# Optimization experiments

Measured on AMD Instinct MI355X. Metric: run time of the kernel, lower is better.

The kernel has to match this reference:

```python
import jax, jax.numpy as jnp
import numpy as np

V, D, M, C, L = 100000, 256, 4096, 4096, 32
PAD = 0
EPS = 1e-8  # torch CosineSimilarity default eps


def setup_inputs() -> dict:
    key = jax.random.key(0)
    ks = jax.random.split(key, 6)
    xs = jax.random.randint(ks[0], (1, L), 0, V)
    mems = jax.random.randint(ks[1], (M, L), 0, V)
    ys = jax.random.randint(ks[2], (1, L), 0, V)
    cands = jax.random.randint(ks[3], (C, L), 0, V)
    lt = jax.random.normal(ks[4], (V, D), dtype=jnp.float32) * 0.02
    lt = lt.at[PAD].set(0.0)  # nn.Embedding padding_idx row is zero
    freqs = jax.random.uniform(ks[5], (V,), dtype=jnp.float32, minval=0.05, maxval=1.0)
    return {"xs": xs, "mems": mems, "ys": ys, "cands": cands, "lt": lt, "freqs": freqs}


def _encode(tokens, lt, freqs):
    # Batched Encoder.forward: freq-weighted average of token embeddings.
    # tokens: [N, L] -> [N, D]
    emb = lt[tokens]                       # [N, L, D] gather
    w = freqs[tokens]                      # [N, L]
    w = w / jnp.linalg.norm(w, axis=1, keepdims=True)  # w * (1 / ||w||)
    return jnp.einsum('nl,nld->nd', w, emb)


def reference(xs, mems, ys, cands, lt, freqs):
    xs_emb = _encode(xs, lt, freqs)                                   # [1, D]
    mems_enc = jnp.concatenate([_encode(mems, lt, freqs), xs_emb], 0)  # [M+1, D]
    # cosine similarity of xs_emb (broadcast) against each memory row
    an = jnp.maximum(jnp.linalg.norm(xs_emb, axis=1), EPS)            # [1]
    bn = jnp.maximum(jnp.linalg.norm(mems_enc, axis=1), EPS)          # [M+1]
    cos = (mems_enc @ xs_emb[0]) / (an * bn)                          # [M+1]
    att = jax.nn.softmax(cos)[None, :]                                # [1, M+1]
    lhs_emb = att @ mems_enc                                          # [1, D]
    ys_emb = _encode(ys, lt, freqs)                                   # [1, D]
    cand_emb = _encode(cands, lt, freqs)                              # [C, D]
    # torch.cat of lhs_emb repeated (1 + C) times; ys then cand encodings
    xs_out = jnp.tile(lhs_emb, (cands.shape[0] + 1, 1))               # [C+1, D]
    ys_out = jnp.concatenate([ys_emb, cand_emb], axis=0)              # [C+1, D]
    return xs_out, ys_out
```

## Files before the change

### kernel.cpp

```cpp
#include <hip/hip_runtime.h>

#define V_ 100000
#define D_ 256
#define M_ 4096
#define C_ 4096
#define L_ 32
#define ROWS_MEMS (M_ + 1)
#define NTASK (1 + M_ + 1 + C_)

__global__ __launch_bounds__(256) void encode_all(
    const int* __restrict__ xs, const int* __restrict__ mems,
    const int* __restrict__ ys, const int* __restrict__ cands,
    const float* __restrict__ lt, const float* __restrict__ freqs,
    float* __restrict__ mems_enc,
    float* __restrict__ out_ys)
{
    const int wave = threadIdx.x >> 6;
    const int lane = threadIdx.x & 63;
    const int rt = blockIdx.x * 4 + wave;
    if (rt >= NTASK) return;

    const int* tok_ptr;
    float* dst;
    if (rt == 0) {
        tok_ptr = xs;
        dst = mems_enc + (size_t)M_ * D_;
    } else if (rt <= M_) {
        tok_ptr = mems + (size_t)(rt - 1) * L_;
        dst = mems_enc + (size_t)(rt - 1) * D_;
    } else if (rt == M_ + 1) {
        tok_ptr = ys;
        dst = out_ys;
    } else {
        const int c = rt - (M_ + 2);
        tok_ptr = cands + (size_t)c * L_;
        dst = out_ys + (size_t)(c + 1) * D_;
    }

    int tok = 0;
    float w = 0.0f;
    if (lane < L_) {
        tok = tok_ptr[lane];
        w = freqs[tok];
    }
    float s = w * w;
    #pragma unroll
    for (int off = 32; off >= 1; off >>= 1) s += __shfl_down(s, off, 64);
    const float norm = sqrtf(__shfl(s, 0, 64));
    const float wn = w / norm;

    const int d0 = lane * 4;
    float4 acc = make_float4(0.f, 0.f, 0.f, 0.f);
    #pragma unroll
    for (int l = 0; l < L_; ++l) {
        const int t = __shfl(tok, l, 64);
        const float wl = __shfl(wn, l, 64);
        const float4 v = *reinterpret_cast<const float4*>(lt + (size_t)t * D_ + d0);
        acc.x += wl * v.x;
        acc.y += wl * v.y;
        acc.z += wl * v.z;
        acc.w += wl * v.w;
    }
    *reinterpret_cast<float4*>(dst + d0) = acc;
}

__global__ __launch_bounds__(256) void dots_kernel(
    const float* __restrict__ enc, float* __restrict__ dots,
    float* __restrict__ norms2)
{
    __shared__ float sp[4], sq[4];
    const int i = blockIdx.x;
    const int t = threadIdx.x;
    const float r = enc[(size_t)i * D_ + t];
    const float x = enc[(size_t)M_ * D_ + t];
    float p = r * x;
    float q = r * r;
    #pragma unroll
    for (int off = 32; off >= 1; off >>= 1) {
        p += __shfl_down(p, off, 64);
        q += __shfl_down(q, off, 64);
    }
    const int wave = t >> 6, lane = t & 63;
    if (lane == 0) { sp[wave] = p; sq[wave] = q; }
    __syncthreads();
    if (t == 0) {
        dots[i]   = sp[0] + sp[1] + sp[2] + sp[3];
        norms2[i] = sq[0] + sq[1] + sq[2] + sq[3];
    }
}

__global__ __launch_bounds__(1024) void softmax_kernel(
    const float* __restrict__ dots, const float* __restrict__ norms2,
    float* __restrict__ att)
{
    __shared__ float red[16];
    const int t = threadIdx.x;
    const int wave = t >> 6, lane = t & 63;

    const float an = fmaxf(sqrtf(norms2[M_]), 1e-8f);

    float cosv[5];
    int cnt = 0;
    float mx = -1e30f;
    for (int i = t; i < ROWS_MEMS; i += 1024) {
        const float bn = fmaxf(sqrtf(norms2[i]), 1e-8f);
        const float c = dots[i] / (an * bn);
        cosv[cnt++] = c;
        mx = fmaxf(mx, c);
    }
    #pragma unroll
    for (int off = 32; off >= 1; off >>= 1) mx = fmaxf(mx, __shfl_down(mx, off, 64));
    if (lane == 0) red[wave] = mx;
    __syncthreads();
    if (t < 16) {
        float m = red[t];
        #pragma unroll
        for (int off = 8; off >= 1; off >>= 1) m = fmaxf(m, __shfl_down(m, off, 16));
        if (t == 0) red[0] = m;
    }
    __syncthreads();
    mx = red[0];
    __syncthreads();

    float s = 0.f;
    for (int k = 0; k < cnt; ++k) { cosv[k] = expf(cosv[k] - mx); s += cosv[k]; }
    #pragma unroll
    for (int off = 32; off >= 1; off >>= 1) s += __shfl_down(s, off, 64);
    if (lane == 0) red[wave] = s;
    __syncthreads();
    if (t < 16) {
        float m = red[t];
        #pragma unroll
        for (int off = 8; off >= 1; off >>= 1) m += __shfl_down(m, off, 16);
        if (t == 0) red[0] = m;
    }
    __syncthreads();
    const float inv = 1.0f / red[0];

    cnt = 0;
    for (int i = t; i < ROWS_MEMS; i += 1024) att[i] = cosv[cnt++] * inv;
}

__global__ __launch_bounds__(256) void lhs_kernel(
    const float* __restrict__ enc, const float* __restrict__ att,
    float* __restrict__ lhs)
{
    const int d = threadIdx.x;
    const int i0 = blockIdx.x * 64;
    const int i1 = min(i0 + 64, ROWS_MEMS);
    float acc = 0.f;
    for (int i = i0; i < i1; ++i) acc += att[i] * enc[(size_t)i * D_ + d];
    atomicAdd(&lhs[d], acc);
}

__global__ __launch_bounds__(256) void tile_kernel(
    const float* __restrict__ lhs, float* __restrict__ out_xs)
{
    out_xs[(size_t)blockIdx.x * D_ + threadIdx.x] = lhs[threadIdx.x];
}

extern "C" void kernel_launch(void* const* d_in, const int* in_sizes, int n_in,
                              void* d_out, int out_size, void* d_ws, size_t ws_size,
                              hipStream_t stream) {
    const int*   xs    = (const int*)d_in[0];
    const int*   mems  = (const int*)d_in[1];
    const int*   ys    = (const int*)d_in[2];
    const int*   cands = (const int*)d_in[3];
    const float* lt    = (const float*)d_in[4];
    const float* freqs = (const float*)d_in[5];

    float* out    = (float*)d_out;
    float* out_xs = out;
    float* out_ys = out + (size_t)ROWS_MEMS * D_;

    float* enc    = (float*)d_ws;
    float* dots   = enc + (size_t)ROWS_MEMS * D_;
    float* norms2 = dots + ROWS_MEMS;
    float* att    = norms2 + ROWS_MEMS;
    float* lhs    = att + ROWS_MEMS;

    hipMemsetAsync(lhs, 0, D_ * sizeof(float), stream);

    encode_all<<<(NTASK + 3) / 4, 256, 0, stream>>>(xs, mems, ys, cands, lt, freqs,
                                                    enc, out_ys);
    dots_kernel<<<ROWS_MEMS, 256, 0, stream>>>(enc, dots, norms2);
    softmax_kernel<<<1, 1024, 0, stream>>>(dots, norms2, att);
    lhs_kernel<<<(ROWS_MEMS + 63) / 64, 256, 0, stream>>>(enc, att, lhs);
    tile_kernel<<<ROWS_MEMS, 256, 0, stream>>>(lhs, out_xs);
}
```

Baseline: 208.9 us.

## Fuse cosine scoring and softmax exponent into encoder, drop max-subtraction and atomics

Each memory-row wave recomputes the xs encoding locally and computes the dot product, norms and exp(cos) right after encoding. This removes the separate dots and softmax kernels along with their global round trips. Because cosine values are bounded in [-1,1], the softmax max-subtraction is dropped. Normalization moves into a chunked weighted-sum kernel plus a final tile kernel that divides by the global sum, replacing the atomic accumulation and the memset. The cost is that every memory wave does an extra 32-row gather for xs, and only 16 blocks perform the weighted reduction over 4097 rows, which limits parallelism in that stage.

```diff
diff --git a/kernel.cpp b/kernel.cpp
--- a/kernel.cpp
+++ b/kernel.cpp
@@ -7,156 +7,116 @@
 #define L_ 32
 #define ROWS_MEMS (M_ + 1)
 #define NTASK (1 + M_ + 1 + C_)
+#define NCHUNK 16
 
-__global__ __launch_bounds__(256) void encode_all(
+__device__ __forceinline__ float wave_allreduce_sum(float v) {
+    #pragma unroll
+    for (int off = 32; off >= 1; off >>= 1) v += __shfl_xor(v, off, 64);
+    return v;
+}
+
+__global__ __launch_bounds__(256) void encode_att(
     const int* __restrict__ xs, const int* __restrict__ mems,
     const int* __restrict__ ys, const int* __restrict__ cands,
     const float* __restrict__ lt, const float* __restrict__ freqs,
-    float* __restrict__ mems_enc,
+    float* __restrict__ enc,
+    float* __restrict__ att,
     float* __restrict__ out_ys)
 {
     const int wave = threadIdx.x >> 6;
     const int lane = threadIdx.x & 63;
     const int rt = blockIdx.x * 4 + wave;
     if (rt >= NTASK) return;
+    const int d0 = lane * 4;
 
-    const int* tok_ptr;
-    float* dst;
+    const int* tok_ptr; float* dst; int ai = -1;
     if (rt == 0) {
-        tok_ptr = xs;
-        dst = mems_enc + (size_t)M_ * D_;
+        tok_ptr = xs;  dst = enc + (size_t)M_ * D_;  ai = M_;
     } else if (rt <= M_) {
         tok_ptr = mems + (size_t)(rt - 1) * L_;
-        dst = mems_enc + (size_t)(rt - 1) * D_;
+        dst = enc + (size_t)(rt - 1) * D_;  ai = rt - 1;
     } else if (rt == M_ + 1) {
-        tok_ptr = ys;
-        dst = out_ys;
+        tok_ptr = ys;  dst = out_ys;
     } else {
         const int c = rt - (M_ + 2);
         tok_ptr = cands + (size_t)c * L_;
         dst = out_ys + (size_t)(c + 1) * D_;
     }
 
-    int tok = 0;
-    float w = 0.0f;
-    if (lane < L_) {
-        tok = tok_ptr[lane];
-        w = freqs[tok];
-    }
-    float s = w * w;
-    #pragma unroll
-    for (int off = 32; off >= 1; off >>= 1) s += __shfl_down(s, off, 64);
-    const float norm = sqrtf(__shfl(s, 0, 64));
-    const float wn = w / norm;
+    int tok = 0; float w = 0.f;
+    if (lane < L_) { tok = tok_ptr[lane]; w = freqs[tok]; }
+    const float s2 = wave_allreduce_sum(w * w);
+    const float wn = w / sqrtf(s2);
 
-    const int d0 = lane * 4;
     float4 acc = make_float4(0.f, 0.f, 0.f, 0.f);
     #pragma unroll
     for (int l = 0; l < L_; ++l) {
         const int t = __shfl(tok, l, 64);
         const float wl = __shfl(wn, l, 64);
         const float4 v = *reinterpret_cast<const float4*>(lt + (size_t)t * D_ + d0);
-        acc.x += wl * v.x;
-        acc.y += wl * v.y;
-        acc.z += wl * v.z;
-        acc.w += wl * v.w;
+        acc.x += wl * v.x; acc.y += wl * v.y; acc.z += wl * v.z; acc.w += wl * v.w;
     }
     *reinterpret_cast<float4*>(dst + d0) = acc;
-}
 
-__global__ __launch_bounds__(256) void dots_kernel(
-    const float* __restrict__ enc, float* __restrict__ dots,
-    float* __restrict__ norms2)
-{
-    __shared__ float sp[4], sq[4];
-    const int i = blockIdx.x;
-    const int t = threadIdx.x;
-    const float r = enc[(size_t)i * D_ + t];
-    const float x = enc[(size_t)M_ * D_ + t];
-    float p = r * x;
-    float q = r * r;
-    #pragma unroll
-    for (int off = 32; off >= 1; off >>= 1) {
-        p += __shfl_down(p, off, 64);
-        q += __shfl_down(q, off, 64);
-    }
-    const int wave = t >> 6, lane = t & 63;
-    if (lane == 0) { sp[wave] = p; sq[wave] = q; }
-    __syncthreads();
-    if (t == 0) {
-        dots[i]   = sp[0] + sp[1] + sp[2] + sp[3];
-        norms2[i] = sq[0] + sq[1] + sq[2] + sq[3];
+    if (ai >= 0) {
+        int txs = 0; float wxs = 0.f;
+        if (lane < L_) { txs = xs[lane]; wxs = freqs[txs]; }
+        const float sx = wave_allreduce_sum(wxs * wxs);
+        const float wnx = wxs / sqrtf(sx);
+        float4 xf = make_float4(0.f, 0.f, 0.f, 0.f);
+        #pragma unroll
+        for (int l = 0; l < L_; ++l) {
+            const int t = __shfl(txs, l, 64);
+            const float wl = __shfl(wnx, l, 64);
+            const float4 v = *reinterpret_cast<const float4*>(lt + (size_t)t * D_ + d0);
+            xf.x += wl * v.x; xf.y += wl * v.y; xf.z += wl * v.z; xf.w += wl * v.w;
+        }
+        const float an2 = wave_allreduce_sum(xf.x*xf.x + xf.y*xf.y + xf.z*xf.z + xf.w*xf.w);
+        const float d  = wave_allreduce_sum(acc.x*xf.x + acc.y*xf.y + acc.z*xf.z + acc.w*xf.w);
+        const float q  = wave_allreduce_sum(acc.x*acc.x + acc.y*acc.y + acc.z*acc.z + acc.w*acc.w);
+        if (lane == 0) {
+            const float an = fmaxf(sqrtf(an2), 1e-8f);
+            const float bn = fmaxf(sqrtf(q),  1e-8f);
+            att[ai] = expf(d / (an * bn));
+        }
     }
 }
 
-__global__ __launch_bounds__(1024) void softmax_kernel(
-    const float* __restrict__ dots, const float* __restrict__ norms2,
-    float* __restrict__ att)
+__global__ __launch_bounds__(256) void lhs_partial(
+    const float* __restrict__ enc, const float* __restrict__ att,
+    float* __restrict__ part,
+    float* __restrict__ gsum)
 {
-    __shared__ float red[16];
     const int t = threadIdx.x;
-    const int wave = t >> 6, lane = t & 63;
-
-    const float an = fmaxf(sqrtf(norms2[M_]), 1e-8f);
-
-    float cosv[5];
-    int cnt = 0;
-    float mx = -1e30f;
-    for (int i = t; i < ROWS_MEMS; i += 1024) {
-        const float bn = fmaxf(sqrtf(norms2[i]), 1e-8f);
-        const float c = dots[i] / (an * bn);
-        cosv[cnt++] = c;
-        mx = fmaxf(mx, c);
+    if (blockIdx.x < NCHUNK) {
+        const int i0 = blockIdx.x * 256;
+        const int i1 = (blockIdx.x == NCHUNK - 1) ? ROWS_MEMS : i0 + 256;
+        float a = 0.f;
+        for (int i = i0; i < i1; ++i) a += att[i] * enc[(size_t)i * D_ + t];
+        part[(size_t)blockIdx.x * D_ + t] = a;
+    } else {
+        __shared__ float red[4];
+        float s = 0.f;
+        for (int i = t; i < ROWS_MEMS; i += 256) s += att[i];
+        s = wave_allreduce_sum(s);
+        const int wave = t >> 6, lane = t & 63;
+        if (lane == 0) red[wave] = s;
+        __syncthreads();
+        if (t == 0) *gsum = red[0] + red[1] + red[2] + red[3];
     }
-    #pragma unroll
-    for (int off = 32; off >= 1; off >>= 1) mx = fmaxf(mx, __shfl_down(mx, off, 64));
-    if (lane == 0) red[wave] = mx;
-    __syncthreads();
-    if (t < 16) {
-        float m = red[t];
-        #pragma unroll
-        for (int off = 8; off >= 1; off >>= 1) m = fmaxf(m, __shfl_down(m, off, 16));
-        if (t == 0) red[0] = m;
-    }
-    __syncthreads();
-    mx = red[0];
-    __syncthreads();
-
-    float s = 0.f;
-    for (int k = 0; k < cnt; ++k) { cosv[k] = expf(cosv[k] - mx); s += cosv[k]; }
-    #pragma unroll
-    for (int off = 32; off >= 1; off >>= 1) s += __shfl_down(s, off, 64);
-    if (lane == 0) red[wave] = s;
-    __syncthreads();
-    if (t < 16) {
-        float m = red[t];
-        #pragma unroll
-        for (int off = 8; off >= 1; off >>= 1) m += __shfl_down(m, off, 16);
-        if (t == 0) red[0] = m;
-    }
-    __syncthreads();
-    const float inv = 1.0f / red[0];
-
-    cnt = 0;
-    for (int i = t; i < ROWS_MEMS; i += 1024) att[i] = cosv[cnt++] * inv;
 }
 
-__global__ __launch_bounds__(256) void lhs_kernel(
-    const float* __restrict__ enc, const float* __restrict__ att,
-    float* __restrict__ lhs)
+__global__ __launch_bounds__(256) void tile_out(
+    const float* __restrict__ part, const float* __restrict__ gsum,
+    float* __restrict__ out_xs)
 {
-    const int d = threadIdx.x;
-    const int i0 = blockIdx.x * 64;
-    const int i1 = min(i0 + 64, ROWS_MEMS);
-    float acc = 0.f;
-    for (int i = i0; i < i1; ++i) acc += att[i] * enc[(size_t)i * D_ + d];
-    atomicAdd(&lhs[d], acc);
-}
-
-__global__ __launch_bounds__(256) void tile_kernel(
-    const float* __restrict__ lhs, float* __restrict__ out_xs)
-{
-    out_xs[(size_t)blockIdx.x * D_ + threadIdx.x] = lhs[threadIdx.x];
+    const int t = threadIdx.x;
+    float a = 0.f;
+    #pragma unroll
+    for (int k = 0; k < NCHUNK; ++k) a += part[(size_t)k * D_ + t];
+    const float val = a / gsum[0];
+    for (int r = blockIdx.x; r < ROWS_MEMS; r += gridDim.x)
+        out_xs[(size_t)r * D_ + t] = val;
 }
 
 extern "C" void kernel_launch(void* const* d_in, const int* in_sizes, int n_in,
@@ -173,18 +133,13 @@
     float* out_xs = out;
     float* out_ys = out + (size_t)ROWS_MEMS * D_;
 
-    float* enc    = (float*)d_ws;
-    float* dots   = enc + (size_t)ROWS_MEMS * D_;
-    float* norms2 = dots + ROWS_MEMS;
-    float* att    = norms2 + ROWS_MEMS;
-    float* lhs    = att + ROWS_MEMS;
+    float* enc  = (float*)d_ws;
+    float* att  = enc + (size_t)ROWS_MEMS * D_;
+    float* part = att + ROWS_MEMS;
+    float* gsum = part + (size_t)NCHUNK * D_;
 
-    hipMemsetAsync(lhs, 0, D_ * sizeof(float), stream);
-
-    encode_all<<<(NTASK + 3) / 4, 256, 0, stream>>>(xs, mems, ys, cands, lt, freqs,
-                                                    enc, out_ys);
-    dots_kernel<<<ROWS_MEMS, 256, 0, stream>>>(enc, dots, norms2);
-    softmax_kernel<<<1, 1024, 0, stream>>>(dots, norms2, att);
-    lhs_kernel<<<(ROWS_MEMS + 63) / 64, 256, 0, stream>>>(enc, att, lhs);
-    tile_kernel<<<ROWS_MEMS, 256, 0, stream>>>(lhs, out_xs);
+    encode_att<<<(NTASK + 3) / 4, 256, 0, stream>>>(xs, mems, ys, cands, lt, freqs,
+                                                    enc, att, out_ys);
+    lhs_partial<<<NCHUNK + 1, 256, 0, stream>>>(enc, att, part, gsum);
+    tile_out<<<1024, 256, 0, stream>>>(part, gsum, out_xs);
 }
```

Measured after the change: 237.0 us. 13.5% more time.
